# Performance work log

Measured on AMD Instinct MI355X. Metric: run time of the kernel, lower is better.

Reference implementation:

```python
import jax, jax.numpy as jnp
import numpy as np

INF = 100000000.0
TOPK = 27


def _box_iou(a, b):
    # a: [N,4] (x1,y1,x2,y2), b: [G,4] -> iou [N,G]
    area_a = (a[:, 2] - a[:, 0]) * (a[:, 3] - a[:, 1])
    area_b = (b[:, 2] - b[:, 0]) * (b[:, 3] - b[:, 1])
    lt = jnp.maximum(a[:, None, :2], b[None, :, :2])
    rb = jnp.minimum(a[:, None, 2:], b[None, :, 2:])
    wh = jnp.clip(rb - lt, 0.0)
    inter = wh[..., 0] * wh[..., 1]
    union = area_a[:, None] + area_b[None, :] - inter
    return inter / union, union


def _assign_one(anchors, gts, tokens):
    # anchors [N,4], gts [G,4], tokens [G,T]
    N = anchors.shape[0]
    G = gts.shape[0]
    ious, _ = _box_iou(anchors, gts)  # [N,G]

    a_cx = (anchors[:, 2] + anchors[:, 0]) * 0.5
    a_cy = (anchors[:, 3] + anchors[:, 1]) * 0.5
    g_cx = (gts[:, 2] + gts[:, 0]) * 0.5
    g_cy = (gts[:, 3] + gts[:, 1]) * 0.5

    # pairwise center distance [N,G]
    dist = jnp.sqrt((a_cx[:, None] - g_cx[None, :]) ** 2 +
                    (a_cy[:, None] - g_cy[None, :]) ** 2)

    # topk nearest anchors per gt (smallest distance) -> idxs [G,TOPK]
    _, topk_idxs = jax.lax.top_k(-dist.T, TOPK)

    # candidate ious [G,TOPK]
    cand = jnp.take_along_axis(ious.T, topk_idxs, axis=1)
    iou_mean = cand.mean(axis=1)
    iou_std = cand.std(axis=1, ddof=1)  # torch.std is unbiased
    is_pos = cand >= (iou_mean + iou_std)[:, None]

    # center-inside-gt check [G,TOPK]
    ax = a_cx[topk_idxs]
    ay = a_cy[topk_idxs]
    l = ax - gts[:, 0:1]
    t = ay - gts[:, 1:2]
    r = gts[:, 2:3] - ax
    b = gts[:, 3:4] - ay
    is_in_gts = jnp.minimum(jnp.minimum(l, t), jnp.minimum(r, b)) > 0.01
    is_pos = is_pos & is_in_gts

    # scatter candidate ious into flat [G*N] buffer of -INF (indices are unique)
    flat_idx = (jnp.arange(G)[:, None] * N + topk_idxs).reshape(-1)
    vals = ious.T.reshape(-1)[flat_idx]
    scat = jnp.where(is_pos.reshape(-1), vals, -INF)
    ious_inf = jnp.full((G * N,), -INF, dtype=ious.dtype).at[flat_idx].set(scat)
    ious_inf = ious_inf.reshape(G, N).T  # [N,G]

    anchors_to_gt_values = ious_inf.max(axis=1)          # [N]
    anchors_to_gt_indexs = ious_inf.argmax(axis=1)       # [N]

    matched_gts = gts[anchors_to_gt_indexs]              # [N,4]

    T = tokens.shape[1]
    unmatched = jnp.zeros((T,), tokens.dtype).at[-1].set(1.0)
    token_labels = jnp.where((anchors_to_gt_values == -INF)[:, None],
                             unmatched[None, :],
                             tokens[anchors_to_gt_indexs])  # [N,T]
    return anchors_to_gt_values, anchors_to_gt_indexs, matched_gts, token_labels


def setup_inputs() -> dict:
    key = jax.random.key(0)
    k1, k2, k3, k4, k5 = jax.random.split(key, 5)
    B, N, G, T = 8, 100000, 64, 256
    # anchors: valid x1<x2, y1<y2 boxes on a ~1024px canvas
    a_c = jax.random.uniform(k1, (B, N, 2), jnp.float32, 0.0, 1024.0)
    a_wh = jax.random.uniform(k2, (B, N, 2), jnp.float32, 8.0, 128.0)
    anchor_boxes = jnp.concatenate([a_c - a_wh / 2, a_c + a_wh / 2], axis=-1)
    g_c = jax.random.uniform(k3, (B, G, 2), jnp.float32, 0.0, 1024.0)
    g_wh = jax.random.uniform(k4, (B, G, 2), jnp.float32, 64.0, 512.0)
    gt_boxes = jnp.concatenate([g_c - g_wh / 2, g_c + g_wh / 2], axis=-1)
    token_map = jax.random.uniform(k5, (B, G, T), jnp.float32)
    return {"anchor_boxes": anchor_boxes, "gt_boxes": gt_boxes,
            "token_map": token_map}


def reference(anchor_boxes, gt_boxes, token_map):
    return jax.vmap(_assign_one)(anchor_boxes, gt_boxes, token_map)
```

## Files before the change

### kernel.cpp

```cpp
#include <hip/hip_runtime.h>
#include <cstdint>

constexpr int B = 8, N = 100000, G = 64, T = 256, TOPK = 27;
constexpr int BN = B * N;
constexpr int CAP = 2048;
#define NEG_INF_VAL (-100000000.0f)

__global__ __launch_bounds__(256) void atss_prep_kernel(
    const float* __restrict__ anchors, float2* __restrict__ ctr,
    unsigned long long* __restrict__ best)
{
#pragma clang fp contract(off)
  int i = blockIdx.x * 256 + threadIdx.x;
  if (i < BN) {
    best[i] = 0ULL;
    float4 ab = ((const float4*)anchors)[i];
    ctr[i] = make_float2((ab.z + ab.x) * 0.5f, (ab.w + ab.y) * 0.5f);
  }
}

__global__ __launch_bounds__(256) void atss_assign_kernel(
    const float* __restrict__ anchors,
    const float2* __restrict__ ctr,
    const float* __restrict__ gts,
    unsigned long long* __restrict__ best)
{
#pragma clang fp contract(off)
  __shared__ float s_d[CAP];
  __shared__ int   s_i[CAP];
  __shared__ int   s_cnt;
  __shared__ int   s_sel[TOPK];
  __shared__ float s_iou[TOPK];
  __shared__ int   s_in[TOPK];
  __shared__ float s_thresh;

  const int bg  = blockIdx.x;
  const int b   = bg / G;
  const int g   = bg % G;
  const int tid = threadIdx.x;

  const float4 gbox = ((const float4*)gts)[bg];
  const float g_cx = (gbox.z + gbox.x) * 0.5f;
  const float g_cy = (gbox.w + gbox.y) * 0.5f;

  const float4*  abase = (const float4*)(anchors + (size_t)b * N * 4);
  const float2*  cbase = ctr + (size_t)b * N;

  float thr = 24.0f;
  int M = 0;
  for (int attempt = 0; attempt < 8; ++attempt) {
    if (tid == 0) s_cnt = 0;
    __syncthreads();
    for (int n = tid; n < N; n += 256) {
      float2 c = cbase[n];
      float dx = c.x - g_cx, dy = c.y - g_cy;
      float d = __fsqrt_rn(__fmul_rn(dx, dx) + __fmul_rn(dy, dy));
      if (d < thr) {
        int p = atomicAdd(&s_cnt, 1);
        if (p < CAP) { s_d[p] = d; s_i[p] = n; }
      }
    }
    __syncthreads();
    int cnt = s_cnt;
    __syncthreads();
    if (cnt >= TOPK && cnt <= CAP) { M = cnt; break; }
    thr = (cnt < TOPK) ? thr * 4.0f : thr * 0.5f;
  }

  for (int s = tid; s < M; s += 256) {
    unsigned long long pk_s =
        ((unsigned long long)__float_as_uint(s_d[s]) << 20) |
        (unsigned long long)(unsigned)s_i[s];
    int rank = 0;
    for (int j = 0; j < M; ++j) {
      unsigned long long pk_j =
          ((unsigned long long)__float_as_uint(s_d[j]) << 20) |
          (unsigned long long)(unsigned)s_i[j];
      rank += (pk_j < pk_s) ? 1 : 0;
    }
    if (rank < TOPK) s_sel[rank] = s_i[s];
  }
  __syncthreads();

  if (tid < TOPK) {
    int a = s_sel[tid];
    float4 ab = abase[a];
    float area_a = __fmul_rn(ab.z - ab.x, ab.w - ab.y);
    float area_b = __fmul_rn(gbox.z - gbox.x, gbox.w - gbox.y);
    float ltx = fmaxf(ab.x, gbox.x), lty = fmaxf(ab.y, gbox.y);
    float rbx = fminf(ab.z, gbox.z), rby = fminf(ab.w, gbox.w);
    float w = fmaxf(rbx - ltx, 0.0f), h = fmaxf(rby - lty, 0.0f);
    float inter = __fmul_rn(w, h);
    float uni = (area_a + area_b) - inter;
    s_iou[tid] = inter / uni;
    float acx = (ab.z + ab.x) * 0.5f, acy = (ab.w + ab.y) * 0.5f;
    float l = acx - gbox.x, t = acy - gbox.y;
    float r = gbox.z - acx, bt = gbox.w - acy;
    float mn = fminf(fminf(l, t), fminf(r, bt));
    s_in[tid] = (mn > 0.01f) ? 1 : 0;
  }
  __syncthreads();

  if (tid == 0) {
    float sum = 0.0f;
    for (int k = 0; k < TOPK; ++k) sum += s_iou[k];
    float mean = sum / (float)TOPK;
    float vs = 0.0f;
    for (int k = 0; k < TOPK; ++k) {
      float d = s_iou[k] - mean;
      vs += __fmul_rn(d, d);
    }
    float sd = __fsqrt_rn(vs / (float)(TOPK - 1));
    s_thresh = mean + sd;
  }
  __syncthreads();

  if (tid < TOPK) {
    float iou = s_iou[tid];
    if (s_in[tid] && iou >= s_thresh) {
      unsigned long long pk =
          ((unsigned long long)__float_as_uint(iou) << 32) |
          (unsigned long long)(0xFFFFFFFFu - (unsigned)g);
      atomicMax(&best[(size_t)b * N + s_sel[tid]], pk);
    }
  }
}

__global__ __launch_bounds__(256) void atss_post_kernel(
    const unsigned long long* __restrict__ best,
    const float* __restrict__ gts,
    float* __restrict__ out,
    int* __restrict__ rowbuf)
{
  const int i = blockIdx.x * 256 + threadIdx.x;
  unsigned long long p = best[i];
  const int b_ = i / N;
  int g = 0;
  float val = NEG_INF_VAL;
  if (p != 0ULL) {
    g   = (int)(0xFFFFFFFFu - (unsigned)(p & 0xFFFFFFFFULL));
    val = __uint_as_float((unsigned)(p >> 32));
  }
  const int row = b_ * G + g;

  out[i] = val;
  out[(size_t)BN + i] = (float)g;
  ((float4*)(out + (size_t)2 * BN))[i] = ((const float4*)gts)[row];
  rowbuf[i] = (p != 0ULL) ? row : -1;
}

constexpr int TW_BLOCKS = 2048;
constexpr int ROWS_PER_WAVE = (BN + 8191) / 8192;

__global__ __launch_bounds__(256) void atss_tok_kernel(
    const int* __restrict__ rowbuf,
    const float* __restrict__ tokens,
    float* __restrict__ out_tok)
{
  const int wv   = (blockIdx.x * 256 + threadIdx.x) >> 6;
  const int lane = threadIdx.x & 63;
  const float4* tok4 = (const float4*)tokens;
  float4* o4 = (float4*)out_tok;

  const int r0 = wv * ROWS_PER_WAVE;
  const int r1 = (r0 + ROWS_PER_WAVE < BN) ? r0 + ROWS_PER_WAVE : BN;
#pragma unroll 2
  for (int row = r0; row < r1; ++row) {
    int r = rowbuf[row];
    float4 t;
    if (r >= 0) {
      t = tok4[(size_t)r * 64 + lane];
    } else {
      t = make_float4(0.0f, 0.0f, 0.0f, (lane == 63) ? 1.0f : 0.0f);
    }
    o4[(size_t)row * 64 + lane] = t;
  }
}

extern "C" void kernel_launch(void* const* d_in, const int* in_sizes, int n_in,
                              void* d_out, int out_size, void* d_ws, size_t ws_size,
                              hipStream_t stream) {
  const float* anchors = (const float*)d_in[0];
  const float* gts     = (const float*)d_in[1];
  const float* tokens  = (const float*)d_in[2];
  float* out = (float*)d_out;

  unsigned long long* best = (unsigned long long*)d_ws;
  float2* ctr = (float2*)((char*)d_ws + sizeof(unsigned long long) * (size_t)BN);
  int* rowbuf = (int*)((char*)d_ws + (sizeof(unsigned long long) + sizeof(float2)) * (size_t)BN);

  atss_prep_kernel<<<(BN + 255) / 256, 256, 0, stream>>>(anchors, ctr, best);
  atss_assign_kernel<<<B * G, 256, 0, stream>>>(anchors, ctr, gts, best);
  atss_post_kernel<<<BN / 256, 256, 0, stream>>>(best, gts, out, rowbuf);
  atss_tok_kernel<<<TW_BLOCKS, 256, 0, stream>>>(rowbuf, tokens, out + (size_t)6 * BN);
}
```

Measured before the change: 979.7 us.

## Split token gather into bulk constant fill plus sparse matched-row fixup

```diff
diff --git a/kernel.cpp b/kernel.cpp
--- a/kernel.cpp
+++ b/kernel.cpp
@@ -4,14 +4,16 @@
 constexpr int B = 8, N = 100000, G = 64, T = 256, TOPK = 27;
 constexpr int BN = B * N;
 constexpr int CAP = 2048;
+constexpr int MAXM = B * G * TOPK;
 #define NEG_INF_VAL (-100000000.0f)
 
 __global__ __launch_bounds__(256) void atss_prep_kernel(
     const float* __restrict__ anchors, float2* __restrict__ ctr,
-    unsigned long long* __restrict__ best)
+    unsigned long long* __restrict__ best, int* __restrict__ mcnt)
 {
 #pragma clang fp contract(off)
   int i = blockIdx.x * 256 + threadIdx.x;
+  if (i == 0) *mcnt = 0;
   if (i < BN) {
     best[i] = 0ULL;
     float4 ab = ((const float4*)anchors)[i];
@@ -130,7 +132,8 @@
     const unsigned long long* __restrict__ best,
     const float* __restrict__ gts,
     float* __restrict__ out,
-    int* __restrict__ rowbuf)
+    int* __restrict__ mcnt,
+    int2* __restrict__ mlist)
 {
   const int i = blockIdx.x * 256 + threadIdx.x;
   unsigned long long p = best[i];
@@ -146,35 +149,38 @@
   out[i] = val;
   out[(size_t)BN + i] = (float)g;
   ((float4*)(out + (size_t)2 * BN))[i] = ((const float4*)gts)[row];
-  rowbuf[i] = (p != 0ULL) ? row : -1;
-}
-
-constexpr int TW_BLOCKS = 2048;
-constexpr int ROWS_PER_WAVE = (BN + 8191) / 8192;
-
-__global__ __launch_bounds__(256) void atss_tok_kernel(
-    const int* __restrict__ rowbuf,
+  if (p != 0ULL) {
+    int s = atomicAdd(mcnt, 1);
+    mlist[s] = make_int2(i, row);
+  }
+}
+
+constexpr long long TOK4 = (long long)BN * 64;
+constexpr int TB_BLOCKS = 8192;
+
+__global__ __launch_bounds__(256) void atss_tok_bulk_kernel(
+    float* __restrict__ out_tok)
+{
+  const long long flat = (long long)blockIdx.x * 256 + threadIdx.x;
+  const long long stride = (long long)TB_BLOCKS * 256;
+  const float4 t = make_float4(0.0f, 0.0f, 0.0f,
+                               ((flat & 63) == 63) ? 1.0f : 0.0f);
+  float4* o4 = (float4*)out_tok;
+  for (long long i = flat; i < TOK4; i += stride) o4[i] = t;
+}
+
+__global__ __launch_bounds__(256) void atss_fix_kernel(
+    const int* __restrict__ mcnt,
+    const int2* __restrict__ mlist,
     const float* __restrict__ tokens,
     float* __restrict__ out_tok)
 {
-  const int wv   = (blockIdx.x * 256 + threadIdx.x) >> 6;
+  const int s    = (blockIdx.x * 256 + threadIdx.x) >> 6;
   const int lane = threadIdx.x & 63;
-  const float4* tok4 = (const float4*)tokens;
-  float4* o4 = (float4*)out_tok;
-
-  const int r0 = wv * ROWS_PER_WAVE;
-  const int r1 = (r0 + ROWS_PER_WAVE < BN) ? r0 + ROWS_PER_WAVE : BN;
-#pragma unroll 2
-  for (int row = r0; row < r1; ++row) {
-    int r = rowbuf[row];
-    float4 t;
-    if (r >= 0) {
-      t = tok4[(size_t)r * 64 + lane];
-    } else {
-      t = make_float4(0.0f, 0.0f, 0.0f, (lane == 63) ? 1.0f : 0.0f);
-    }
-    o4[(size_t)row * 64 + lane] = t;
-  }
+  if (s >= *mcnt) return;
+  int2 e = mlist[s];
+  ((float4*)(out_tok + (size_t)e.x * T))[lane] =
+      ((const float4*)tokens)[(size_t)e.y * 64 + lane];
 }
 
 extern "C" void kernel_launch(void* const* d_in, const int* in_sizes, int n_in,
@@ -184,13 +190,17 @@
   const float* gts     = (const float*)d_in[1];
   const float* tokens  = (const float*)d_in[2];
   float* out = (float*)d_out;
-
-  unsigned long long* best = (unsigned long long*)d_ws;
-  float2* ctr = (float2*)((char*)d_ws + sizeof(unsigned long long) * (size_t)BN);
-  int* rowbuf = (int*)((char*)d_ws + (sizeof(unsigned long long) + sizeof(float2)) * (size_t)BN);
-
-  atss_prep_kernel<<<(BN + 255) / 256, 256, 0, stream>>>(anchors, ctr, best);
+  float* out_tok = out + (size_t)6 * BN;
+
+  char* ws = (char*)d_ws;
+  unsigned long long* best = (unsigned long long*)ws;
+  float2* ctr  = (float2*)(ws + 8 * (size_t)BN);
+  int*    mcnt = (int*)(ws + 16 * (size_t)BN);
+  int2*   mlist = (int2*)(ws + 16 * (size_t)BN + 256);
+
+  atss_prep_kernel<<<(BN + 255) / 256, 256, 0, stream>>>(anchors, ctr, best, mcnt);
   atss_assign_kernel<<<B * G, 256, 0, stream>>>(anchors, ctr, gts, best);
-  atss_post_kernel<<<BN / 256, 256, 0, stream>>>(best, gts, out, rowbuf);
-  atss_tok_kernel<<<TW_BLOCKS, 256, 0, stream>>>(rowbuf, tokens, out + (size_t)6 * BN);
-}
+  atss_post_kernel<<<BN / 256, 256, 0, stream>>>(best, gts, out, mcnt, mlist);
+  atss_tok_bulk_kernel<<<TB_BLOCKS, 256, 0, stream>>>(out_tok);
+  atss_fix_kernel<<<(MAXM + 3) / 4, 256, 0, stream>>>(mcnt, mlist, tokens, out_tok);
+}
```

Result: no change. 978.1 us (-0.2%).
